# Optimization experiments

Hardware: AMD Instinct MI355X
Metric: run time of the kernel (lower is better)

Reference implementation:

```python
import jax, jax.numpy as jnp
import numpy as np

B, N, M, C = 64, 16384, 64, 512
OUT = 3 * M + 6  # 198
EPS = 1e-8


def setup_inputs() -> dict:
    key = jax.random.key(0)
    k0, k1, k2, k3 = jax.random.split(key, 4)
    x = jax.random.normal(k0, (B, C), jnp.float32)
    # previous write weighting: a valid distribution over N rows
    w_prev = jax.nn.softmax(jax.random.normal(k1, (B, N), jnp.float32), axis=-1)
    memory = jax.random.normal(k2, (B, N, M), jnp.float32) * 0.1
    W = jax.random.normal(k3, (C, OUT), jnp.float32) * (1.0 / np.sqrt(C))
    b = jnp.zeros((OUT,), jnp.float32)
    return {"x": x, "w_prev": w_prev, "memory": memory, "W": W, "b": b}


def _address(memory, k, beta, g, s, gamma, w_prev):
    # content addressing: cosine similarity between key k [B,M] and memory [B,N,M]
    dot = jnp.einsum('bnm,bm->bn', memory, k)
    denom = jnp.linalg.norm(memory, axis=-1) * jnp.linalg.norm(k, axis=-1, keepdims=True) + EPS
    w_c = jax.nn.softmax(beta * dot / denom, axis=-1)          # [B,N]
    # interpolation gate
    w_g = g * w_c + (1.0 - g) * w_prev                          # [B,N]
    # circular convolution over shifts [-1, 0, +1]
    w_s = (s[:, 0:1] * jnp.roll(w_g, -1, axis=-1)
           + s[:, 1:2] * w_g
           + s[:, 2:3] * jnp.roll(w_g, 1, axis=-1))             # [B,N]
    # sharpening
    w_sharp = jnp.power(w_s + EPS, gamma)                       # gamma [B,1]
    return w_sharp / jnp.sum(w_sharp, axis=-1, keepdims=True)


def reference(x, w_prev, memory, W, b):
    proj = x @ W + b                                            # [B, 3M+6]
    k = proj[:, :M]
    beta = jax.nn.softplus(proj[:, M:M + 1])
    g = jax.nn.sigmoid(proj[:, M + 1:M + 2])
    s = jax.nn.softmax(proj[:, M + 2:M + 5], axis=-1)
    gamma = 1.0 + jax.nn.softplus(proj[:, M + 5:M + 6])
    e = jax.nn.sigmoid(proj[:, M + 6:M + 6 + M])
    a = proj[:, M + 6 + M:]
    w = _address(memory, k, beta, g, s, gamma, w_prev)          # [B,N]
    # erase-add write: mem' = mem * (1 - w^T e) + w^T a
    erase = jnp.einsum('bn,bm->bnm', w, e)
    add = jnp.einsum('bn,bm->bnm', w, a)
    mem_new = memory * (1.0 - erase) + add
    return proj, w, mem_new
```

## Files before the change

### kernel.cpp

```cpp
#include <hip/hip_runtime.h>
#include <math.h>

#define BB   64
#define NN   16384
#define MM   64
#define CIN  512
#define OUTD 198
#define EPSF 1e-8f

#define NCHUNK (NN / 256)
#define NBLK   (BB * NCHUNK)
#define UPD_BLKS 16384

__device__ inline float softplusf(float v) {
    return v > 20.f ? v : log1pf(expf(v));
}
__device__ inline float sigmoidf(float v) {
    return 1.f / (1.f + expf(-v));
}

__global__ __launch_bounds__(256) void proj_kernel(
    const float* __restrict__ x, const float* __restrict__ W,
    const float* __restrict__ bias, float* __restrict__ out_proj,
    float* __restrict__ scal, float* __restrict__ ea)
{
    const int b = blockIdx.x;
    const int tid = threadIdx.x;
    __shared__ __align__(16) float xs[CIN];
    __shared__ float pr[OUTD];

    for (int c = tid; c < CIN; c += 256) xs[c] = x[b * CIN + c];
    __syncthreads();

    if (tid < OUTD) {
        float acc = bias[tid];
        #pragma unroll 8
        for (int c = 0; c < CIN; ++c)
            acc = fmaf(xs[c], W[c * OUTD + tid], acc);
        out_proj[b * OUTD + tid] = acc;
        pr[tid] = acc;
    }
    __syncthreads();

    if (tid < MM) {
        ea[b * 128 + tid]      = sigmoidf(pr[MM + 6 + tid]);
        ea[b * 128 + 64 + tid] = pr[MM + 6 + MM + tid];
    }
    if (tid == 0) {
        float beta  = softplusf(pr[MM]);
        float g     = sigmoidf(pr[MM + 1]);
        float s0r = pr[MM + 2], s1r = pr[MM + 3], s2r = pr[MM + 4];
        float mx  = fmaxf(s0r, fmaxf(s1r, s2r));
        float e0 = expf(s0r - mx), e1 = expf(s1r - mx), e2 = expf(s2r - mx);
        float inv = 1.f / (e0 + e1 + e2);
        float gamma = 1.f + softplusf(pr[MM + 5]);
        float ksq = 0.f;
        for (int m = 0; m < MM; ++m) ksq += pr[m] * pr[m];
        float* sc = scal + b * 8;
        sc[0] = beta; sc[1] = g;
        sc[2] = e0 * inv; sc[3] = e1 * inv; sc[4] = e2 * inv;
        sc[5] = gamma; sc[6] = sqrtf(ksq);
    }
}

__global__ __launch_bounds__(256) void score_kernel(
    const float* __restrict__ mem, const float* __restrict__ proj,
    const float* __restrict__ scal, float* __restrict__ score,
    float* __restrict__ partials)
{
    const int b     = blockIdx.x >> 6;
    const int chunk = blockIdx.x & 63;
    const int tid   = threadIdx.x;
    const int rowbase = chunk * 256;

    __shared__ __align__(16) float ks[MM];
    __shared__ float rowsc[256];
    __shared__ float red[8];

    if (tid < MM) ks[tid] = proj[b * OUTD + tid];
    __syncthreads();

    const float beta  = scal[b * 8 + 0];
    const float knorm = scal[b * 8 + 6];
    const int sub = tid & 15;
    const int rg  = tid >> 4;
    const float4 kv = *(const float4*)(&ks[sub * 4]);
    const float4* base = (const float4*)(mem + ((size_t)b * NN + rowbase) * MM);

    #pragma unroll
    for (int it = 0; it < 16; ++it) {
        const float4 v = base[(it * 16 + rg) * 16 + sub];
        float dot = v.x * kv.x + v.y * kv.y + v.z * kv.z + v.w * kv.w;
        float nsq = v.x * v.x + v.y * v.y + v.z * v.z + v.w * v.w;
        #pragma unroll
        for (int o = 1; o < 16; o <<= 1) {
            dot += __shfl_xor(dot, o);
            nsq += __shfl_xor(nsq, o);
        }
        if (sub == 0) {
            const float sc = beta * dot / (sqrtf(nsq) * knorm + EPSF);
            score[(size_t)b * NN + rowbase + it * 16 + rg] = sc;
            rowsc[it * 16 + rg] = sc;
        }
    }
    __syncthreads();

    const float sc = rowsc[tid];
    float mv = sc;
    #pragma unroll
    for (int o = 32; o > 0; o >>= 1) mv = fmaxf(mv, __shfl_xor(mv, o));
    const int wid = tid >> 6, lane = tid & 63;
    if (lane == 0) red[wid] = mv;
    __syncthreads();
    if (tid == 0) red[4] = fmaxf(fmaxf(red[0], red[1]), fmaxf(red[2], red[3]));
    __syncthreads();
    const float mb = red[4];

    float ex = expf(sc - mb);
    #pragma unroll
    for (int o = 32; o > 0; o >>= 1) ex += __shfl_xor(ex, o);
    if (lane == 0) red[wid] = ex;
    __syncthreads();
    if (tid == 0) {
        partials[2 * blockIdx.x]     = mb;
        partials[2 * blockIdx.x + 1] = red[0] + red[1] + red[2] + red[3];
    }
}

__global__ __launch_bounds__(64) void combine_kernel(
    const float* __restrict__ partials, float* __restrict__ Mb,
    float* __restrict__ Sb, float* __restrict__ sumW)
{
    const int b = blockIdx.x, t = threadIdx.x;
    const float mb = partials[2 * (b * NCHUNK + t)];
    const float sb = partials[2 * (b * NCHUNK + t) + 1];
    float M = mb;
    #pragma unroll
    for (int o = 32; o > 0; o >>= 1) M = fmaxf(M, __shfl_xor(M, o));
    float contrib = sb * expf(mb - M);
    #pragma unroll
    for (int o = 32; o > 0; o >>= 1) contrib += __shfl_xor(contrib, o);
    if (t == 0) { Mb[b] = M; Sb[b] = contrib; sumW[b] = 0.f; }
}

__global__ __launch_bounds__(256) void sharp_kernel(
    const float* __restrict__ score, const float* __restrict__ w_prev,
    const float* __restrict__ scal, const float* __restrict__ Mb,
    const float* __restrict__ Sb, float* __restrict__ wsharp,
    float* __restrict__ sumW)
{
    const int b     = blockIdx.x >> 6;
    const int chunk = blockIdx.x & 63;
    const int tid   = threadIdx.x;
    const int start = chunk * 256;

    __shared__ float wg[258];
    __shared__ float red[8];

    const float g    = scal[b * 8 + 1];
    const float Mv   = Mb[b];
    const float invS = 1.f / Sb[b];
    const float* scb = score  + (size_t)b * NN;
    const float* wpb = w_prev + (size_t)b * NN;

    for (int i = tid; i < 258; i += 256) {
        const int idx = (start - 1 + i + NN) & (NN - 1);
        const float wc = expf(scb[idx] - Mv) * invS;
        wg[i] = g * wc + (1.f - g) * wpb[idx];
    }
    __syncthreads();

    const float s0 = scal[b * 8 + 2], s1 = scal[b * 8 + 3];
    const float s2 = scal[b * 8 + 4], gamma = scal[b * 8 + 5];
    const float ws  = s0 * wg[tid + 2] + s1 * wg[tid + 1] + s2 * wg[tid];
    const float wsh = powf(ws + EPSF, gamma);
    wsharp[(size_t)b * NN + start + tid] = wsh;

    float sum = wsh;
    #pragma unroll
    for (int o = 32; o > 0; o >>= 1) sum += __shfl_xor(sum, o);
    const int wid = tid >> 6, lane = tid & 63;
    if (lane == 0) red[wid] = sum;
    __syncthreads();
    if (tid == 0) atomicAdd(&sumW[b], red[0] + red[1] + red[2] + red[3]);
}

__global__ __launch_bounds__(256) void update_kernel(
    const float* __restrict__ mem, const float* __restrict__ ea_g,
    const float* __restrict__ wsharp, const float* __restrict__ sumW,
    float* __restrict__ out_w, float* __restrict__ out_mem)
{
    const int blk = UPD_BLKS - 1 - (int)blockIdx.x;
    const int tid = threadIdx.x;
    const int b   = blk >> 8;

    __shared__ __align__(16) float ea[128];
    if (tid < 32) *(float4*)(&ea[tid * 4]) =
        *(const float4*)(&ea_g[b * 128 + tid * 4]);
    __syncthreads();

    const int m = (tid * 4) & 63;
    const float4 e4 = *(const float4*)(&ea[m]);
    const float4 a4 = *(const float4*)(&ea[64 + m]);
    const float invS = 1.0f / sumW[b];
    const size_t base_f = (size_t)blk * 4096;
    const float* wsb = wsharp + (size_t)b * NN;
    float*       owb = out_w  + (size_t)b * NN;

    #pragma unroll
    for (int it = 0; it < 4; ++it) {
        const size_t off = base_f + (size_t)it * 1024 + tid * 4;
        const int n = (int)((off >> 6) & (NN - 1));
        const float w = wsb[n] * invS;
        if ((tid & 15) == 0) owb[n] = w;
        const float4 v = *(const float4*)(mem + off);
        float4 r;
        r.x = v.x * (1.f - w * e4.x) + w * a4.x;
        r.y = v.y * (1.f - w * e4.y) + w * a4.y;
        r.z = v.z * (1.f - w * e4.z) + w * a4.z;
        r.w = v.w * (1.f - w * e4.w) + w * a4.w;
        *(float4*)(out_mem + off) = r;
    }
}

extern "C" void kernel_launch(void* const* d_in, const int* in_sizes, int n_in,
                              void* d_out, int out_size, void* d_ws, size_t ws_size,
                              hipStream_t stream)
{
    const float* x      = (const float*)d_in[0];
    const float* w_prev = (const float*)d_in[1];
    const float* memory = (const float*)d_in[2];
    const float* W      = (const float*)d_in[3];
    const float* bias   = (const float*)d_in[4];

    float* out      = (float*)d_out;
    float* out_proj = out;
    float* out_w    = out + BB * OUTD;
    float* out_mem  = out_w + (size_t)BB * NN;

    float* ws_f     = (float*)d_ws;
    float* score    = ws_f;
    float* wsharp   = score + (size_t)BB * NN;
    float* partials = wsharp + (size_t)BB * NN;
    float* Mb       = partials + 2 * NBLK;
    float* Sb       = Mb + BB;
    float* sumW     = Sb + BB;
    float* scal     = sumW + BB;
    float* ea       = scal + 8 * BB;

    proj_kernel   <<<BB,      256, 0, stream>>>(x, W, bias, out_proj, scal, ea);
    score_kernel  <<<NBLK,    256, 0, stream>>>(memory, out_proj, scal, score, partials);
    combine_kernel<<<BB,       64, 0, stream>>>(partials, Mb, Sb, sumW);
    sharp_kernel  <<<NBLK,    256, 0, stream>>>(score, w_prev, scal, Mb, Sb, wsharp, sumW);
    update_kernel <<<UPD_BLKS,256, 0, stream>>>(memory, ea, wsharp, sumW, out_w, out_mem);
}
```

Measured before the change: 572.8 us.

## Keep scores in registers in score kernel; enlarge update blocks to 256 rows

New measurement: 576.6 us. Within noise of the previous version (+0.7%).

```diff
diff --git a/kernel.cpp b/kernel.cpp
--- a/kernel.cpp
+++ b/kernel.cpp
@@ -10,7 +10,7 @@
 
 #define NCHUNK (NN / 256)
 #define NBLK   (BB * NCHUNK)
-#define UPD_BLKS 16384
+#define UPD_BLKS (BB * 64)
 
 __device__ inline float softplusf(float v) {
     return v > 20.f ? v : log1pf(expf(v));
@@ -72,21 +72,19 @@
     const int chunk = blockIdx.x & 63;
     const int tid   = threadIdx.x;
     const int rowbase = chunk * 256;
-
-    __shared__ __align__(16) float ks[MM];
-    __shared__ float rowsc[256];
-    __shared__ float red[8];
-
-    if (tid < MM) ks[tid] = proj[b * OUTD + tid];
-    __syncthreads();
-
+    const int sub = tid & 15;
+    const int rg  = tid >> 4;
+
+    __shared__ float redm[4];
+    __shared__ float reds[4];
+
+    const float4 kv   = *(const float4*)(&proj[b * OUTD + sub * 4]);
     const float beta  = scal[b * 8 + 0];
     const float knorm = scal[b * 8 + 6];
-    const int sub = tid & 15;
-    const int rg  = tid >> 4;
-    const float4 kv = *(const float4*)(&ks[sub * 4]);
     const float4* base = (const float4*)(mem + ((size_t)b * NN + rowbase) * MM);
 
+    float scr[16];
+    float mv = -INFINITY;
     #pragma unroll
     for (int it = 0; it < 16; ++it) {
         const float4 v = base[(it * 16 + rg) * 16 + sub];
@@ -97,33 +95,29 @@
             dot += __shfl_xor(dot, o);
             nsq += __shfl_xor(nsq, o);
         }
-        if (sub == 0) {
-            const float sc = beta * dot / (sqrtf(nsq) * knorm + EPSF);
-            score[(size_t)b * NN + rowbase + it * 16 + rg] = sc;
-            rowsc[it * 16 + rg] = sc;
-        }
-    }
-    __syncthreads();
-
-    const float sc = rowsc[tid];
-    float mv = sc;
-    #pragma unroll
-    for (int o = 32; o > 0; o >>= 1) mv = fmaxf(mv, __shfl_xor(mv, o));
+        const float sc = beta * dot / (sqrtf(nsq) * knorm + EPSF);
+        scr[it] = sc;
+        mv = fmaxf(mv, sc);
+        if (sub == 0) score[(size_t)b * NN + rowbase + it * 16 + rg] = sc;
+    }
+
+    mv = fmaxf(mv, __shfl_xor(mv, 16));
+    mv = fmaxf(mv, __shfl_xor(mv, 32));
     const int wid = tid >> 6, lane = tid & 63;
-    if (lane == 0) red[wid] = mv;
-    __syncthreads();
-    if (tid == 0) red[4] = fmaxf(fmaxf(red[0], red[1]), fmaxf(red[2], red[3]));
-    __syncthreads();
-    const float mb = red[4];
-
-    float ex = expf(sc - mb);
-    #pragma unroll
-    for (int o = 32; o > 0; o >>= 1) ex += __shfl_xor(ex, o);
-    if (lane == 0) red[wid] = ex;
+    if (lane == 0) redm[wid] = mv;
+    __syncthreads();
+    const float mb = fmaxf(fmaxf(redm[0], redm[1]), fmaxf(redm[2], redm[3]));
+
+    float s = 0.f;
+    #pragma unroll
+    for (int it = 0; it < 16; ++it) s += expf(scr[it] - mb);
+    s += __shfl_xor(s, 16);
+    s += __shfl_xor(s, 32);
+    if (lane == 0) reds[wid] = s;
     __syncthreads();
     if (tid == 0) {
         partials[2 * blockIdx.x]     = mb;
-        partials[2 * blockIdx.x + 1] = red[0] + red[1] + red[2] + red[3];
+        partials[2 * blockIdx.x + 1] = reds[0] + reds[1] + reds[2] + reds[3];
     }
 }
 
@@ -190,36 +184,36 @@
     const float* __restrict__ wsharp, const float* __restrict__ sumW,
     float* __restrict__ out_w, float* __restrict__ out_mem)
 {
-    const int blk = UPD_BLKS - 1 - (int)blockIdx.x;
-    const int tid = threadIdx.x;
-    const int b   = blk >> 8;
-
-    __shared__ __align__(16) float ea[128];
-    if (tid < 32) *(float4*)(&ea[tid * 4]) =
-        *(const float4*)(&ea_g[b * 128 + tid * 4]);
-    __syncthreads();
-
-    const int m = (tid * 4) & 63;
-    const float4 e4 = *(const float4*)(&ea[m]);
-    const float4 a4 = *(const float4*)(&ea[64 + m]);
+    const int blk   = UPD_BLKS - 1 - (int)blockIdx.x;
+    const int b     = blk >> 6;
+    const int chunk = blk & 63;
+    const int tid   = threadIdx.x;
+    const int sub   = tid & 15;
+    const int rg    = tid >> 4;
+
+    const float4 e4 = *(const float4*)(&ea_g[b * 128 + sub * 4]);
+    const float4 a4 = *(const float4*)(&ea_g[b * 128 + 64 + sub * 4]);
     const float invS = 1.0f / sumW[b];
-    const size_t base_f = (size_t)blk * 4096;
-    const float* wsb = wsharp + (size_t)b * NN;
-    float*       owb = out_w  + (size_t)b * NN;
-
-    #pragma unroll
-    for (int it = 0; it < 4; ++it) {
-        const size_t off = base_f + (size_t)it * 1024 + tid * 4;
-        const int n = (int)((off >> 6) & (NN - 1));
-        const float w = wsb[n] * invS;
-        if ((tid & 15) == 0) owb[n] = w;
-        const float4 v = *(const float4*)(mem + off);
+
+    const int n0 = chunk * 256;
+    const float* wsb = wsharp + (size_t)b * NN + n0;
+
+    out_w[(size_t)b * NN + n0 + tid] = wsb[tid] * invS;
+
+    const float4* src = (const float4*)(mem     + ((size_t)b * NN + n0) * MM);
+    float4*       dst = (float4*)      (out_mem + ((size_t)b * NN + n0) * MM);
+
+    #pragma unroll 8
+    for (int it = 0; it < 16; ++it) {
+        const int row = it * 16 + rg;
+        const float w = wsb[row] * invS;
+        const float4 v = src[row * 16 + sub];
         float4 r;
-        r.x = v.x * (1.f - w * e4.x) + w * a4.x;
-        r.y = v.y * (1.f - w * e4.y) + w * a4.y;
-        r.z = v.z * (1.f - w * e4.z) + w * a4.z;
-        r.w = v.w * (1.f - w * e4.w) + w * a4.w;
-        *(float4*)(out_mem + off) = r;
+        r.x = fmaf(-w * e4.x, v.x, fmaf(w, a4.x, v.x));
+        r.y = fmaf(-w * e4.y, v.y, fmaf(w, a4.y, v.y));
+        r.z = fmaf(-w * e4.z, v.z, fmaf(w, a4.z, v.z));
+        r.w = fmaf(-w * e4.w, v.w, fmaf(w, a4.w, v.w));
+        dst[row * 16 + sub] = r;
     }
 }
 
```
